# Kernel optimization log

Measured on AMD Instinct MI355X. Metric: run time of the kernel, lower is better.

## Reference

```python
import jax, jax.numpy as jnp
import numpy as np

NH, NL, NP, GA = 8, 4, 4, 8  # num_heads, num_levels, num_points, grid_align_num
SHAPES = np.array([[128, 128], [64, 64], [32, 32], [16, 16]], dtype=np.int64)  # (W, H) per level


def _grid_sample(img, grid):
    """F.grid_sample bilinear, padding_mode='zeros', align_corners=False.
    img: [N,C,H,W], grid: [N,Hg,Wg,2] in [-1,1] (x,y). Returns [N,C,Hg,Wg]."""
    N, C, H, W = img.shape
    x = (grid[..., 0] + 1.0) * (W * 0.5) - 0.5
    y = (grid[..., 1] + 1.0) * (H * 0.5) - 0.5
    x0 = jnp.floor(x)
    y0 = jnp.floor(y)
    wx = (x - x0)[:, None]  # [N,1,Hg,Wg]
    wy = (y - y0)[:, None]
    x0i = x0.astype(jnp.int32)
    y0i = y0.astype(jnp.int32)
    img_flat = img.reshape(N, C, H * W)
    Hg, Wg = grid.shape[1], grid.shape[2]

    def tap(ix, iy):
        valid = (ix >= 0) & (ix < W) & (iy >= 0) & (iy < H)
        lin = jnp.clip(iy, 0, H - 1) * W + jnp.clip(ix, 0, W - 1)
        v = jnp.take_along_axis(img_flat, lin.reshape(N, 1, Hg * Wg), axis=2)
        return v.reshape(N, C, Hg, Wg) * valid[:, None].astype(img.dtype)

    v00 = tap(x0i, y0i)
    v01 = tap(x0i + 1, y0i)
    v10 = tap(x0i, y0i + 1)
    v11 = tap(x0i + 1, y0i + 1)
    return (v00 * (1 - wx) * (1 - wy) + v01 * wx * (1 - wy)
            + v10 * (1 - wx) * wy + v11 * wx * wy)


def setup_inputs() -> dict:
    key = jax.random.key(0)
    ks = jax.random.split(key, 6)
    bs, nq, E = 2, 16384, 256
    total = int((SHAPES[:, 0] * SHAPES[:, 1]).sum())  # 21760
    query = jax.random.normal(ks[0], (bs, nq, E), jnp.float32)
    value = jax.random.normal(ks[1], (bs, total, NH, E // NH), jnp.float32)
    reference_points = jax.random.uniform(ks[2], (bs, nq, 1, NL * 2), jnp.float32)
    W_off = jax.random.normal(ks[3], (NH * NL * NP * 2, E), jnp.float32) * 0.01
    # structured offset bias per init_weights (directional rays, radius ~ point index)
    thetas = jnp.arange(NH, dtype=jnp.float32) * (2.0 * np.pi / NH)
    gi = jnp.stack([jnp.cos(thetas), jnp.sin(thetas)], -1)  # [NH,2]
    gi = gi / jnp.max(jnp.abs(gi), axis=-1, keepdims=True)
    gi = jnp.tile(gi[:, None, None, :], (1, NL, NP, 1))
    gi = gi * jnp.arange(1, NP + 1, dtype=jnp.float32)[None, None, :, None]
    b_off = gi.reshape(-1)
    W_attn = jax.random.normal(ks[4], (NH * NL * NP, E), jnp.float32) * 0.01
    b_attn = jax.random.normal(ks[5], (NH * NL * NP,), jnp.float32) * 0.01
    return {"query": query, "value": value, "reference_points": reference_points,
            "W_off": W_off, "b_off": b_off, "W_attn": W_attn, "b_attn": b_attn,
            "spatial_shapes": np.asarray(SHAPES)}


def reference(query, value, reference_points, W_off, b_off, W_attn, b_attn, spatial_shapes):
    bs, nq, E = query.shape
    d = E // NH
    shapes = np.asarray(spatial_shapes)  # static [L,2] (W,H)

    # sampling offsets and locations (non-deploy path)
    off = (query @ W_off.T + b_off).reshape(bs, nq, NH, NL * NP * 2)
    ref = jnp.tile(reference_points, (1, 1, NH, NP)).reshape(bs, nq, NH, NL * NP * 2)
    # offset_normalizer: (1/spatial_shapes).repeat(1, NP).flatten() -> layout (l, p, xy)
    norm = jnp.asarray(np.tile(1.0 / shapes.astype(np.float32), (1, NP)).reshape(-1))
    loc = (ref + off * norm) * 2.0 - 1.0  # [bs, nq, NH, NL*NP*2]

    # attention weights: softmax over levels*points, regrouped to (L, G, P) layout
    attn = jax.nn.softmax((query @ W_attn.T + b_attn).reshape(bs, nq, NH, NL * NP), axis=-1)
    attn = (attn.reshape(bs, nq // GA, GA, NH, NL, NP)
            .transpose(0, 3, 1, 4, 2, 5)
            .reshape(bs * NH, 1, nq // GA, NL * GA * NP))

    grids = loc.reshape(bs, nq, NH, NL, NP, 2)
    outs = []
    start = 0
    for lvl in range(NL):
        W_, H_ = int(shapes[lvl, 0]), int(shapes[lvl, 1])
        n = H_ * W_
        v = value[:, start:start + n].transpose(0, 2, 3, 1).reshape(bs * NH, d, H_, W_)
        start += n
        g = grids[:, :, :, lvl].transpose(0, 2, 1, 3, 4).reshape(bs * NH, nq // GA, GA * NP, 2)
        outs.append(_grid_sample(v, g))  # [bs*NH, d, nq//GA, GA*NP]
    samp = jnp.concatenate(outs, axis=-1) * attn  # [bs*NH, d, nq//GA, NL*GA*NP]
    # reduce_sum linear with fixed 0/1 weight == sum over levels and points per group slot
    out = samp.reshape(bs * NH, d, nq // GA, NL, GA, NP).sum(axis=(3, 5))
    return out.reshape(bs, NH * d, nq)
```

## Files before the change

kernel.cpp:

```cpp
#include <hip/hip_runtime.h>
#include <hip/hip_bf16.h>


typedef __attribute__((ext_vector_type(4))) float    float4v;
typedef __attribute__((ext_vector_type(8))) _Float16 half8;
typedef __attribute__((ext_vector_type(4))) _Float16 half4;
typedef __attribute__((ext_vector_type(2))) _Float16 half2v;

#define NQ    16384
#define NTOK  21760
#define NLOG  384

#define N_V4  2785280

union H8 { half8 v; half2v p[4]; };

__global__ __launch_bounds__(256) void convert_kernel(
    const float* __restrict__ val, _Float16* __restrict__ vh) {
  int i = blockIdx.x * 256 + threadIdx.x;
  float4v v = ((const float4v*)val)[i];
  half4 o;
  o[0] = (_Float16)v[0]; o[1] = (_Float16)v[1];
  o[2] = (_Float16)v[2]; o[3] = (_Float16)v[3];
  ((half4*)vh)[i] = o;
}

#define LDSTR 88
__global__ __launch_bounds__(256) void gemm_kernel(
    const float* __restrict__ qf,
    const float* __restrict__ Woff, const float* __restrict__ Wattn,
    const float* __restrict__ boff, const float* __restrict__ battn,
    _Float16* __restrict__ lh) {
  __shared__ _Float16 As[64 * LDSTR];
  __shared__ _Float16 Bs[128 * LDSTR];

  const int tid  = threadIdx.x;
  const int lane = tid & 63;
  const int wv   = tid >> 6;
  const int wm   = wv >> 1, wn = wv & 1;
  const int quad = lane >> 4;
  const int r    = lane & 15;
  const int blockM = blockIdx.x * 64;
  const int n0     = blockIdx.y * 128;

  float4v acc[2][4];
#pragma unroll
  for (int i = 0; i < 2; ++i)
#pragma unroll
    for (int j = 0; j < 4; ++j) acc[i][j] = (float4v){0.f, 0.f, 0.f, 0.f};

  for (int kc = 0; kc < 4; ++kc) {
    const int k0 = kc * 64;
    if (kc) __syncthreads();
#pragma unroll
    for (int it = 0; it < 4; ++it) {
      int idx = it * 256 + tid;
      int row = idx >> 4, k4 = idx & 15;
      float4v v = *(const float4v*)(qf + (size_t)(blockM + row) * 256 + k0 + k4 * 4);
      half4 o;
      o[0] = (_Float16)v[0]; o[1] = (_Float16)v[1];
      o[2] = (_Float16)v[2]; o[3] = (_Float16)v[3];
      *(half4*)&As[row * LDSTR + k4 * 4] = o;
    }
#pragma unroll
    for (int it = 0; it < 8; ++it) {
      int idx = it * 256 + tid;
      int row = idx >> 4, k4 = idx & 15;
      int n = n0 + row;
      const float* src = (n < 256) ? (Woff + (size_t)n * 256)
                                   : (Wattn + (size_t)(n - 256) * 256);
      float4v v = *(const float4v*)(src + k0 + k4 * 4);
      half4 o;
      o[0] = (_Float16)v[0]; o[1] = (_Float16)v[1];
      o[2] = (_Float16)v[2]; o[3] = (_Float16)v[3];
      *(half4*)&Bs[row * LDSTR + k4 * 4] = o;
    }
    __syncthreads();

#pragma unroll
    for (int kf = 0; kf < 2; ++kf) {
      const int ko = kf * 32 + quad * 8;
      half8 af[2], bf[4];
#pragma unroll
      for (int mi = 0; mi < 2; ++mi)
        af[mi] = *(const half8*)&As[(wm * 32 + mi * 16 + r) * LDSTR + ko];
#pragma unroll
      for (int ni = 0; ni < 4; ++ni)
        bf[ni] = *(const half8*)&Bs[(wn * 64 + ni * 16 + r) * LDSTR + ko];
#pragma unroll
      for (int mi = 0; mi < 2; ++mi)
#pragma unroll
        for (int ni = 0; ni < 4; ++ni)
          acc[mi][ni] = __builtin_amdgcn_mfma_f32_16x16x32_f16(af[mi], bf[ni], acc[mi][ni], 0, 0, 0);
    }
  }

#pragma unroll
  for (int mi = 0; mi < 2; ++mi) {
    const int mb = blockM + wm * 32 + mi * 16 + quad * 4;
#pragma unroll
    for (int ni = 0; ni < 4; ++ni) {
      const int n = n0 + wn * 64 + ni * 16 + r;
      const float bias = (n < 256) ? boff[n] : battn[n - 256];
#pragma unroll
      for (int reg = 0; reg < 4; ++reg)
        lh[(size_t)(mb + reg) * NLOG + n] = (_Float16)(acc[mi][ni][reg] + bias);
    }
  }
}

__global__ __launch_bounds__(256) void sample_kernel(
    const _Float16* __restrict__ vh, const float* __restrict__ refp,
    const _Float16* __restrict__ lh, float* __restrict__ out) {
  const int qt = blockIdx.x, h = blockIdx.y, b = blockIdx.z;
  const int tid = threadIdx.x;
  const int c4 = tid & 3;
  const int qi = tid >> 2;
  const int q  = qt * 64 + qi;
  const size_t bq = (size_t)b * NQ + q;
  const _Float16* lg = lh + bq * NLOG;

  float offf[32];
#pragma unroll
  for (int i = 0; i < 4; ++i) {
    half8 oh = *(const half8*)(lg + h * 32 + i * 8);
#pragma unroll
    for (int j = 0; j < 8; ++j) offf[i * 8 + j] = (float)oh[j];
  }
  float al[16];
#pragma unroll
  for (int i = 0; i < 2; ++i) {
    half8 ah = *(const half8*)(lg + 256 + h * 16 + i * 8);
#pragma unroll
    for (int j = 0; j < 8; ++j) al[i * 8 + j] = (float)ah[j];
  }
  float mx = -1e30f;
#pragma unroll
  for (int i = 0; i < 16; ++i) mx = fmaxf(mx, al[i]);
  float ssum = 0.f;
#pragma unroll
  for (int i = 0; i < 16; ++i) {
    float e = __expf(al[i] - mx);
    al[i] = e;
    ssum += e;
  }
  const float inv = 1.0f / ssum;

  float4v rp0 = *(const float4v*)(refp + bq * 8);
  float4v rp1 = *(const float4v*)(refp + bq * 8 + 4);
  const float rpx[4] = {rp0[0], rp0[2], rp1[0], rp1[2]};
  const float rpy[4] = {rp0[1], rp0[3], rp1[1], rp1[3]};

  const _Float16* vb = vh + (size_t)b * NTOK * 256 + h * 32 + c4 * 8;
  float4v acc0 = (float4v){0.f, 0.f, 0.f, 0.f};
  float4v acc1 = (float4v){0.f, 0.f, 0.f, 0.f};

  const int base[4] = {0, 16384, 20480, 21504};

#pragma unroll
  for (int l = 0; l < 4; ++l) {
    const int   W  = 128 >> l;
    const float fW = (float)W;
    const _Float16* vlev = vb + (size_t)base[l] * 256;
    half2v accl[4];
#pragma unroll
    for (int j = 0; j < 4; ++j) accl[j] = (half2v){(_Float16)0, (_Float16)0};
#pragma unroll
    for (int p = 0; p < 4; ++p) {
      const float a  = al[l * 4 + p] * inv;
      const float ox = offf[l * 8 + p * 2];
      const float oy = offf[l * 8 + p * 2 + 1];
      const float x = rpx[p] * fW + ox - 0.5f;
      const float y = rpy[p] * fW + oy - 0.5f;
      const float xf = floorf(x), yf = floorf(y);
      const float fx = x - xf, fy = y - yf;
      const int ix = (int)xf, iy = (int)yf;
      const int ix0 = min(max(ix, 0), W - 1);
      const int ix1 = min(max(ix + 1, 0), W - 1);
      const int iy0 = min(max(iy, 0), W - 1);
      const int iy1 = min(max(iy + 1, 0), W - 1);
      const float wx0 = ((unsigned)ix       < (unsigned)W) ? 1.f - fx : 0.f;
      const float wx1 = ((unsigned)(ix + 1) < (unsigned)W) ? fx       : 0.f;
      const float wy0 = ((unsigned)iy       < (unsigned)W) ? 1.f - fy : 0.f;
      const float wy1 = ((unsigned)(iy + 1) < (unsigned)W) ? fy       : 0.f;
      const _Float16 w00 = (_Float16)(a * wx0 * wy0);
      const _Float16 w01 = (_Float16)(a * wx1 * wy0);
      const _Float16 w10 = (_Float16)(a * wx0 * wy1);
      const _Float16 w11 = (_Float16)(a * wx1 * wy1);
      const half2v h00 = (half2v){w00, w00};
      const half2v h01 = (half2v){w01, w01};
      const half2v h10 = (half2v){w10, w10};
      const half2v h11 = (half2v){w11, w11};
      const _Float16* r0 = vlev + (size_t)(iy0 * W) * 256;
      const _Float16* r1 = vlev + (size_t)(iy1 * W) * 256;
      H8 t00, t01, t10, t11;
      t00.v = *(const half8*)(r0 + ix0 * 256);
      t01.v = *(const half8*)(r0 + ix1 * 256);
      t10.v = *(const half8*)(r1 + ix0 * 256);
      t11.v = *(const half8*)(r1 + ix1 * 256);
#pragma unroll
      for (int j = 0; j < 4; ++j) {
        accl[j] += h00 * t00.p[j] + h01 * t01.p[j]
                 + h10 * t10.p[j] + h11 * t11.p[j];
      }
    }
    acc0[0] += (float)accl[0][0]; acc0[1] += (float)accl[0][1];
    acc0[2] += (float)accl[1][0]; acc0[3] += (float)accl[1][1];
    acc1[0] += (float)accl[2][0]; acc1[1] += (float)accl[2][1];
    acc1[2] += (float)accl[3][0]; acc1[3] += (float)accl[3][1];
  }

  __shared__ float sm[32][65];
#pragma unroll
  for (int j = 0; j < 4; ++j) {
    sm[c4 * 8 + j][qi]     = acc0[j];
    sm[c4 * 8 + 4 + j][qi] = acc1[j];
  }
  __syncthreads();
  const size_t obase = ((size_t)b * 256 + h * 32) * NQ + qt * 64;
#pragma unroll
  for (int i = 0; i < 8; ++i) {
    const int idx = i * 256 + tid;
    const int c = idx >> 6, qq = idx & 63;
    out[obase + (size_t)c * NQ + qq] = sm[c][qq];
  }
}

extern "C" void kernel_launch(void* const* d_in, const int* in_sizes, int n_in,
                              void* d_out, int out_size, void* d_ws, size_t ws_size,
                              hipStream_t stream) {
  const float* query = (const float*)d_in[0];
  const float* value = (const float*)d_in[1];
  const float* refp  = (const float*)d_in[2];
  const float* Woff  = (const float*)d_in[3];
  const float* boff  = (const float*)d_in[4];
  const float* Wattn = (const float*)d_in[5];
  const float* battn = (const float*)d_in[6];
  float* out = (float*)d_out;

  char* ws = (char*)d_ws;
  _Float16* vh = (_Float16*)ws;
  _Float16* lh = (_Float16*)(ws + 22282240);

  convert_kernel<<<10880, 256, 0, stream>>>(value, vh);
  gemm_kernel<<<dim3(512, 3), 256, 0, stream>>>(query, Woff, Wattn, boff, battn, lh);
  sample_kernel<<<dim3(256, 8, 2), 256, 0, stream>>>(vh, refp, lh, out);
}
```

Baseline: 239.1 us.

## Pre-convert weights to fp16, widen GEMM tile to full N, reorder sample grid

The convert kernel now also casts the offset and attention weight matrices to fp16 once. The GEMM uses 128-row blocks of 512 threads covering all 384 output columns, so the query tile is loaded and converted once instead of three times. B fragments are read straight from global fp16 weights rather than staged through LDS. The sample kernel grid is reordered so the head/batch index varies fastest, giving neighbouring blocks locality on the same query rows. The trade-offs are fewer GEMM blocks (256), higher register pressure from 24 accumulators per thread, and uncached-through-LDS global B loads.

```diff
diff --git a/kernel.cpp b/kernel.cpp
--- a/kernel.cpp
+++ b/kernel.cpp
@@ -16,91 +16,90 @@
 union H8 { half8 v; half2v p[4]; };
 
 __global__ __launch_bounds__(256) void convert_kernel(
-    const float* __restrict__ val, _Float16* __restrict__ vh) {
+    const float* __restrict__ val,
+    const float* __restrict__ Woff, const float* __restrict__ Wattn,
+    _Float16* __restrict__ vh, _Float16* __restrict__ wh) {
   int i = blockIdx.x * 256 + threadIdx.x;
-  float4v v = ((const float4v*)val)[i];
+  float4v v;
+  half4* dst;
+  if (i < N_V4) {
+    v = ((const float4v*)val)[i];
+    dst = ((half4*)vh) + i;
+  } else {
+    int j = i - N_V4;
+    int n = j >> 6;
+    int k4 = j & 63;
+    const float* src = (n < 256) ? (Woff + (size_t)n * 256)
+                                 : (Wattn + (size_t)(n - 256) * 256);
+    v = *(const float4v*)(src + k4 * 4);
+    dst = ((half4*)wh) + j;
+  }
   half4 o;
   o[0] = (_Float16)v[0]; o[1] = (_Float16)v[1];
   o[2] = (_Float16)v[2]; o[3] = (_Float16)v[3];
-  ((half4*)vh)[i] = o;
-}
-
-#define LDSTR 88
-__global__ __launch_bounds__(256) void gemm_kernel(
-    const float* __restrict__ qf,
-    const float* __restrict__ Woff, const float* __restrict__ Wattn,
+  *dst = o;
+}
+
+#define ALD 136
+__global__ __launch_bounds__(512, 2) void gemm_kernel(
+    const float* __restrict__ qf, const _Float16* __restrict__ wh,
     const float* __restrict__ boff, const float* __restrict__ battn,
     _Float16* __restrict__ lh) {
-  __shared__ _Float16 As[64 * LDSTR];
-  __shared__ _Float16 Bs[128 * LDSTR];
+  __shared__ _Float16 As[128 * ALD];
 
   const int tid  = threadIdx.x;
   const int lane = tid & 63;
   const int wv   = tid >> 6;
-  const int wm   = wv >> 1, wn = wv & 1;
+  const int wm   = wv >> 2, wn = wv & 3;
   const int quad = lane >> 4;
   const int r    = lane & 15;
-  const int blockM = blockIdx.x * 64;
-  const int n0     = blockIdx.y * 128;
-
-  float4v acc[2][4];
-#pragma unroll
-  for (int i = 0; i < 2; ++i)
-#pragma unroll
-    for (int j = 0; j < 4; ++j) acc[i][j] = (float4v){0.f, 0.f, 0.f, 0.f};
-
-  for (int kc = 0; kc < 4; ++kc) {
-    const int k0 = kc * 64;
+  const int blockM = blockIdx.x * 128;
+
+  float4v acc[4][6];
+#pragma unroll
+  for (int i = 0; i < 4; ++i)
+#pragma unroll
+    for (int j = 0; j < 6; ++j) acc[i][j] = (float4v){0.f, 0.f, 0.f, 0.f};
+
+  for (int kc = 0; kc < 2; ++kc) {
+    const int k0 = kc * 128;
     if (kc) __syncthreads();
 #pragma unroll
-    for (int it = 0; it < 4; ++it) {
-      int idx = it * 256 + tid;
-      int row = idx >> 4, k4 = idx & 15;
+    for (int it = 0; it < 8; ++it) {
+      int idx = it * 512 + tid;
+      int row = idx >> 5, k4 = idx & 31;
       float4v v = *(const float4v*)(qf + (size_t)(blockM + row) * 256 + k0 + k4 * 4);
       half4 o;
       o[0] = (_Float16)v[0]; o[1] = (_Float16)v[1];
       o[2] = (_Float16)v[2]; o[3] = (_Float16)v[3];
-      *(half4*)&As[row * LDSTR + k4 * 4] = o;
-    }
-#pragma unroll
-    for (int it = 0; it < 8; ++it) {
-      int idx = it * 256 + tid;
-      int row = idx >> 4, k4 = idx & 15;
-      int n = n0 + row;
-      const float* src = (n < 256) ? (Woff + (size_t)n * 256)
-                                   : (Wattn + (size_t)(n - 256) * 256);
-      float4v v = *(const float4v*)(src + k0 + k4 * 4);
-      half4 o;
-      o[0] = (_Float16)v[0]; o[1] = (_Float16)v[1];
-      o[2] = (_Float16)v[2]; o[3] = (_Float16)v[3];
-      *(half4*)&Bs[row * LDSTR + k4 * 4] = o;
+      *(half4*)&As[row * ALD + k4 * 4] = o;
     }
     __syncthreads();
 
 #pragma unroll
-    for (int kf = 0; kf < 2; ++kf) {
-      const int ko = kf * 32 + quad * 8;
-      half8 af[2], bf[4];
-#pragma unroll
-      for (int mi = 0; mi < 2; ++mi)
-        af[mi] = *(const half8*)&As[(wm * 32 + mi * 16 + r) * LDSTR + ko];
-#pragma unroll
-      for (int ni = 0; ni < 4; ++ni)
-        bf[ni] = *(const half8*)&Bs[(wn * 64 + ni * 16 + r) * LDSTR + ko];
-#pragma unroll
-      for (int mi = 0; mi < 2; ++mi)
-#pragma unroll
-        for (int ni = 0; ni < 4; ++ni)
+    for (int kt = 0; kt < 4; ++kt) {
+      const int ko = kt * 32 + quad * 8;
+      half8 af[4], bf[6];
+#pragma unroll
+      for (int mi = 0; mi < 4; ++mi)
+        af[mi] = *(const half8*)&As[(wm * 64 + mi * 16 + r) * ALD + ko];
+#pragma unroll
+      for (int ni = 0; ni < 6; ++ni)
+        bf[ni] = *(const half8*)(wh + (size_t)(wn * 96 + ni * 16 + r) * 256 + k0 + ko);
+#pragma unroll
+      for (int mi = 0; mi < 4; ++mi)
+#pragma unroll
+        for (int ni = 0; ni < 6; ++ni)
           acc[mi][ni] = __builtin_amdgcn_mfma_f32_16x16x32_f16(af[mi], bf[ni], acc[mi][ni], 0, 0, 0);
     }
   }
 
 #pragma unroll
-  for (int mi = 0; mi < 2; ++mi) {
-    const int mb = blockM + wm * 32 + mi * 16 + quad * 4;
-#pragma unroll
-    for (int ni = 0; ni < 4; ++ni) {
-      const int n = n0 + wn * 64 + ni * 16 + r;
+  for (int mi = 0; mi < 4; ++mi) {
+    const int mb = blockM + wm * 64 + mi * 16 + quad * 4;
+#pragma unroll
+    for (int ni = 0; ni < 6; ++ni) {
+      const int n = wn * 96 + ni * 16 + r;
       const float bias = (n < 256) ? boff[n] : battn[n - 256];
 #pragma unroll
       for (int reg = 0; reg < 4; ++reg)
@@ -112,7 +111,9 @@
 __global__ __launch_bounds__(256) void sample_kernel(
     const _Float16* __restrict__ vh, const float* __restrict__ refp,
     const _Float16* __restrict__ lh, float* __restrict__ out) {
-  const int qt = blockIdx.x, h = blockIdx.y, b = blockIdx.z;
+  const int hb = blockIdx.x;
+  const int h = hb & 7, b = hb >> 3;
+  const int qt = blockIdx.y;
   const int tid = threadIdx.x;
   const int c4 = tid & 3;
   const int qi = tid >> 2;
@@ -240,9 +241,10 @@
 
   char* ws = (char*)d_ws;
   _Float16* vh = (_Float16*)ws;
-  _Float16* lh = (_Float16*)(ws + 22282240);
-
-  convert_kernel<<<10880, 256, 0, stream>>>(value, vh);
-  gemm_kernel<<<dim3(512, 3), 256, 0, stream>>>(query, Woff, Wattn, boff, battn, lh);
-  sample_kernel<<<dim3(256, 8, 2), 256, 0, stream>>>(vh, refp, lh, out);
-}
+  _Float16* wh = (_Float16*)(ws + 22282240);
+  _Float16* lh = (_Float16*)(ws + 22478848);
+
+  convert_kernel<<<10976, 256, 0, stream>>>(value, Woff, Wattn, vh, wh);
+  gemm_kernel<<<256, 512, 0, stream>>>(query, wh, boff, battn, lh);
+  sample_kernel<<<dim3(16, 256), 256, 0, stream>>>(vh, refp, lh, out);
+}
```

Result: slower. 245.2 us (+2.5%).
